# Kernel tuning notes

Hardware: AMD Instinct MI355X
Metric: run time of the kernel (lower is better)

Reference implementation:

```python
import jax, jax.numpy as jnp
import numpy as np

B, S, D_MODEL = 8, 2048, 512
G, V = 2, 320          # num_groups, num_vars
CV_DIM = 256 // G      # proj_dim // num_groups = 128
TAU = 2.0


def setup_inputs() -> dict:
    key = jax.random.key(0)
    k1, k2, k3, k4, k5 = jax.random.split(key, 5)
    hidden_states = jax.random.normal(k1, (B, S, D_MODEL), dtype=jnp.float32)
    # Linear(d_model -> G*V); store as (in, out) for direct matmul
    W = jax.random.normal(k2, (D_MODEL, G * V), dtype=jnp.float32) * (1.0 / np.sqrt(D_MODEL))
    b = jax.random.normal(k3, (G * V,), dtype=jnp.float32) * 0.01
    codevectors = jax.random.normal(k4, (1, G * V, CV_DIM), dtype=jnp.float32)
    # pre-sampled Gumbel(0,1) noise, shape (B*S*G, V)
    u = jax.random.uniform(k5, (B * S * G, V), dtype=jnp.float32,
                           minval=1e-10, maxval=1.0)
    gumbels = -jnp.log(-jnp.log(u))
    return {"hidden_states": hidden_states, "W": W, "b": b,
            "codevectors": codevectors, "gumbels": gumbels}


def reference(hidden_states, W, b, codevectors, gumbels):
    Bs, Ss, _ = hidden_states.shape
    N = Bs * Ss
    # weight projection: (B,S,D) @ (D,G*V) -> (B,S,G*V)
    logits = hidden_states @ W + b
    logits = logits.reshape(N * G, V).astype(jnp.float32)

    # gumbel-softmax, hard=True with straight-through
    y_soft = jax.nn.softmax((logits + gumbels) / TAU, axis=-1)  # (N*G, V)
    idx = jnp.argmax(y_soft, axis=-1)
    y_hard = jax.nn.one_hot(idx, V, dtype=y_soft.dtype)
    codevector_probs = y_hard - jax.lax.stop_gradient(y_soft) + y_soft

    # perplexity from the (noise-free) soft distribution
    soft_dist = jax.nn.softmax(logits.reshape(N, G, V), axis=-1)
    marginal = soft_dist.mean(axis=0)                            # (G, V)
    perplexity = jnp.exp(-jnp.sum(marginal * jnp.log(marginal + 1e-7),
                                  axis=-1)).sum()

    # codebook lookup as weighted sum (equivalent to one-hot gather)
    cv = codevectors.reshape(G, V, CV_DIM)
    probs = codevector_probs.reshape(N, G, V)
    out = jnp.einsum('ngv,gvd->ngd', probs, cv)                  # (N, G, d)
    out = out.reshape(Bs, Ss, G * CV_DIM)
    return out, perplexity
```

## Files before the change

kernel.cpp:

```cpp
#include <hip/hip_runtime.h>

#define M_ROWS 16384
#define K_DIM  512
#define N_COLS 640
#define V_CODES 320
#define CV_DIM 128
#define LSTRIDE 330

typedef _Float16 half8 __attribute__((ext_vector_type(8)));
typedef _Float16 half4v __attribute__((ext_vector_type(4)));
typedef float floatx4 __attribute__((ext_vector_type(4)));

__device__ inline void gll16(const void* g, void* l) {
    __builtin_amdgcn_global_load_lds(
        (const __attribute__((address_space(1))) void*)g,
        (__attribute__((address_space(3))) void*)l, 16, 0, 0);
}

__global__ __launch_bounds__(256)
void prepW(const float* __restrict__ W, _Float16* __restrict__ Wt,
           float* __restrict__ marginal) {
    __shared__ float tile[32][33];
    const int b = blockIdx.x, t = threadIdx.x;
    if (b == 320) {
        for (int i = t; i < 640; i += 256) marginal[i] = 0.f;
        return;
    }
    const int n0 = (b % 20) * 32, k0 = (b / 20) * 32;
    {
        const int kk = t >> 3, nn4 = (t & 7) << 2;
        const float4 w = *(const float4*)(W + (size_t)(k0 + kk) * 640 + n0 + nn4);
        tile[kk][nn4 + 0] = w.x; tile[kk][nn4 + 1] = w.y;
        tile[kk][nn4 + 2] = w.z; tile[kk][nn4 + 3] = w.w;
    }
    __syncthreads();
    {
        const int nn = t >> 3, kk4 = (t & 7) << 2;
        half4v h = {(_Float16)tile[kk4 + 0][nn], (_Float16)tile[kk4 + 1][nn],
                    (_Float16)tile[kk4 + 2][nn], (_Float16)tile[kk4 + 3][nn]};
        *(half4v*)(Wt + (size_t)(n0 + nn) * 512 + k0 + kk4) = h;
    }
}

union SMemG {
    struct { _Float16 Bs[2][320 * 32]; _Float16 As[2][64 * 32]; } g;
    _Float16 L[64 * LSTRIDE];
};

__global__ __launch_bounds__(256, 3)
void fused(const float* __restrict__ A, const _Float16* __restrict__ Bt,
           const float* __restrict__ bias, const float* __restrict__ gum,
           const float* __restrict__ cv, float* __restrict__ out,
           float* __restrict__ marginal) {
    __shared__ SMemG sm;
    __shared__ float smarg[320];
    const int t = threadIdx.x;
    const int wave = t >> 6, lane = t & 63;
    const int bm = blockIdx.x, g = blockIdx.y;
    const int mi = wave;
    const int c = lane & 15, kq = lane >> 4;

    for (int i = t; i < 320; i += 256) smarg[i] = 0.f;

    floatx4 acc[20];
#pragma unroll
    for (int nt = 0; nt < 20; ++nt) acc[nt] = (floatx4){0.f, 0.f, 0.f, 0.f};

    const int am = t >> 2, ad = t & 3;
    const int a_wr = am * 64 + ((ad ^ (am & 3)) << 4);
    const float* Aptr = A + (size_t)(bm * 64 + am) * 512 + ad * 8;

    const _Float16* Bg = Bt + (size_t)g * V_CODES * K_DIM;

    auto STAGE = [&](int buf, int k0) {
        const float4 av0 = *(const float4*)(Aptr + k0);
        const float4 av1 = *(const float4*)(Aptr + k0 + 4);
#pragma unroll
        for (int s = 0; s < 5; ++s) {
            const int q = t + 256 * s;
            const int n = q >> 2, j = q & 3;
            gll16(Bg + (size_t)n * 512 + k0 + ((j ^ (n & 3)) << 3),
                  (char*)(&sm.g.Bs[buf][0]) + q * 16);
        }
        const half8 h = {(_Float16)av0.x, (_Float16)av0.y, (_Float16)av0.z,
                         (_Float16)av0.w, (_Float16)av1.x, (_Float16)av1.y,
                         (_Float16)av1.z, (_Float16)av1.w};
        *(half8*)((char*)(&sm.g.As[buf][0]) + a_wr) = h;
    };

    STAGE(0, 0);
    __syncthreads();

    for (int kt = 0; kt < 16; ++kt) {
        const int cur = kt & 1;
        if (kt < 15) STAGE(cur ^ 1, (kt + 1) * 32);
        const int ra = mi * 16 + c;
        const half8 af = *(const half8*)((const char*)(&sm.g.As[cur][0]) +
                          ra * 64 + ((kq ^ (ra & 3)) << 4));
#pragma unroll
        for (int nt = 0; nt < 20; ++nt) {
            const int rb = nt * 16 + c;
            const half8 bf = *(const half8*)((const char*)(&sm.g.Bs[cur][0]) +
                              rb * 64 + ((kq ^ (rb & 3)) << 4));
            acc[nt] = __builtin_amdgcn_mfma_f32_16x16x32_f16(af, bf, acc[nt], 0, 0, 0);
        }
        __syncthreads();
    }

    float bcol[20];
#pragma unroll
    for (int nt = 0; nt < 20; ++nt) bcol[nt] = bias[g * V_CODES + nt * 16 + c];
#pragma unroll
    for (int rg = 0; rg < 4; ++rg) {
        const int row = mi * 16 + kq * 4 + rg;
#pragma unroll
        for (int nt = 0; nt < 20; ++nt)
            sm.L[row * LSTRIDE + nt * 16 + c] = (_Float16)(acc[nt][rg] + bcol[nt]);
    }

    float gv[4][20];
#pragma unroll
    for (int rg = 0; rg < 4; ++rg) {
        const int ntok = bm * 64 + mi * 16 + kq * 4 + rg;
        const float* gr = gum + ((size_t)ntok * 2 + g) * V_CODES + c;
#pragma unroll
        for (int nt = 0; nt < 20; ++nt) gv[rg][nt] = gr[nt * 16];
    }

    float mcontrib[20];
#pragma unroll
    for (int nt = 0; nt < 20; ++nt) mcontrib[nt] = 0.f;

#pragma unroll
    for (int rg = 0; rg < 4; ++rg) {
        const int row = mi * 16 + kq * 4 + rg;
        float lg[20];
#pragma unroll
        for (int nt = 0; nt < 20; ++nt)
            lg[nt] = (float)sm.L[row * LSTRIDE + nt * 16 + c];
        float best = -1e30f; int bidx = 0;
#pragma unroll
        for (int nt = 0; nt < 20; ++nt) {
            const float nz = lg[nt] + gv[rg][nt];
            const int v = nt * 16 + c;
            if (nz > best) { best = nz; bidx = v; }
        }
#pragma unroll
        for (int mask = 1; mask <= 8; mask <<= 1) {
            const float ob = __shfl_xor(best, mask);
            const int   oi = __shfl_xor(bidx, mask);
            if (ob > best || (ob == best && oi < bidx)) { best = ob; bidx = oi; }
        }
        float s = 0.f;
#pragma unroll
        for (int nt = 0; nt < 20; ++nt) { lg[nt] = __expf(lg[nt]); s += lg[nt]; }
#pragma unroll
        for (int mask = 1; mask <= 8; mask <<= 1) s += __shfl_xor(s, mask);
        const float inv = 1.f / s;
#pragma unroll
        for (int nt = 0; nt < 20; ++nt) mcontrib[nt] += lg[nt] * inv;
        const int ntok = bm * 64 + row;
        const float4* cvp = (const float4*)(cv + ((size_t)g * V_CODES + bidx) * CV_DIM)
                            + c * 2;
        const float4 v0 = cvp[0], v1 = cvp[1];
        float4* op = (float4*)(out + (size_t)ntok * 256 + g * CV_DIM) + c * 2;
        op[0] = v0; op[1] = v1;
    }

#pragma unroll
    for (int nt = 0; nt < 20; ++nt) {
        mcontrib[nt] += __shfl_xor(mcontrib[nt], 16);
        mcontrib[nt] += __shfl_xor(mcontrib[nt], 32);
    }
    if (lane < 16) {
#pragma unroll
        for (int nt = 0; nt < 20; ++nt)
            atomicAdd(&smarg[nt * 16 + c], mcontrib[nt]);
    }
    __syncthreads();
    for (int i = t; i < 320; i += 256)
        atomicAdd(marginal + g * V_CODES + i, smarg[i]);
}

__global__ __launch_bounds__(640)
void finalize(const float* __restrict__ marginal, float* __restrict__ perp_out) {
    __shared__ float terms[640];
    __shared__ float gsum[2];
    const int t = threadIdx.x;

    const float m = marginal[t] * (1.0f / (float)M_ROWS);
    terms[t] = -m * __logf(m + 1e-7f);
    __syncthreads();

    if (t < 128) {
        const int g = t >> 6, lane = t & 63;
        float e = 0.f;
#pragma unroll
        for (int j = 0; j < 5; ++j) e += terms[g * V_CODES + lane + 64 * j];
#pragma unroll
        for (int off = 32; off; off >>= 1) e += __shfl_down(e, off);
        if (lane == 0) gsum[g] = e;
    }
    __syncthreads();
    if (t == 0) perp_out[0] = __expf(gsum[0]) + __expf(gsum[1]);
}

extern "C" void kernel_launch(void* const* d_in, const int* in_sizes, int n_in,
                              void* d_out, int out_size, void* d_ws, size_t ws_size,
                              hipStream_t stream) {
    (void)in_sizes; (void)n_in; (void)out_size; (void)ws_size;
    const float* hs = (const float*)d_in[0];
    const float* W  = (const float*)d_in[1];
    const float* bi = (const float*)d_in[2];
    const float* cv = (const float*)d_in[3];
    const float* gu = (const float*)d_in[4];
    float* out = (float*)d_out;

    _Float16* Wt       = (_Float16*)d_ws;
    float*    marginal = (float*)(Wt + (size_t)N_COLS * K_DIM);

    prepW<<<321, 256, 0, stream>>>(W, Wt, marginal);
    fused<<<dim3(256, 2), 256, 0, stream>>>(hs, Wt, bi, gu, cv, out, marginal);
    finalize<<<1, 640, 0, stream>>>(marginal, out + (size_t)M_ROWS * 256);
}
```

Measured before the change: 50.72 us.

## Stage gumbel noise through LDS with async loads and keep logits in registers

The epilogue no longer round-trips the biased logits through an fp16 LDS buffer. It uses the accumulator registers directly, which also keeps the logits in full fp32. The gumbel noise was previously loaded with strided per-lane global reads. It is now brought into LDS in two 32-row halves with coalesced 16-byte global_load_lds transfers, and the matching two waves process each half. This is meant to fix the poorly coalesced gumbel reads and drop the LDS logit write and read. In exchange, it serializes the epilogue into two phases with extra barriers, leaving half the waves idle in each phase.

```diff
diff --git a/kernel.cpp b/kernel.cpp
--- a/kernel.cpp
+++ b/kernel.cpp
@@ -5,7 +5,6 @@
 #define N_COLS 640
 #define V_CODES 320
 #define CV_DIM 128
-#define LSTRIDE 330
 
 typedef _Float16 half8 __attribute__((ext_vector_type(8)));
 typedef _Float16 half4v __attribute__((ext_vector_type(4)));
@@ -44,7 +43,7 @@
 
 union SMemG {
     struct { _Float16 Bs[2][320 * 32]; _Float16 As[2][64 * 32]; } g;
-    _Float16 L[64 * LSTRIDE];
+    float gumL[32 * 320];
 };
 
 __global__ __launch_bounds__(256, 3)
@@ -107,77 +106,77 @@
         __syncthreads();
     }
 
-    float bcol[20];
-#pragma unroll
-    for (int nt = 0; nt < 20; ++nt) bcol[nt] = bias[g * V_CODES + nt * 16 + c];
-#pragma unroll
-    for (int rg = 0; rg < 4; ++rg) {
-        const int row = mi * 16 + kq * 4 + rg;
-#pragma unroll
-        for (int nt = 0; nt < 20; ++nt)
-            sm.L[row * LSTRIDE + nt * 16 + c] = (_Float16)(acc[nt][rg] + bcol[nt]);
-    }
-
-    float gv[4][20];
-#pragma unroll
-    for (int rg = 0; rg < 4; ++rg) {
-        const int ntok = bm * 64 + mi * 16 + kq * 4 + rg;
-        const float* gr = gum + ((size_t)ntok * 2 + g) * V_CODES + c;
-#pragma unroll
-        for (int nt = 0; nt < 20; ++nt) gv[rg][nt] = gr[nt * 16];
-    }
-
-    float mcontrib[20];
-#pragma unroll
-    for (int nt = 0; nt < 20; ++nt) mcontrib[nt] = 0.f;
-
-#pragma unroll
-    for (int rg = 0; rg < 4; ++rg) {
-        const int row = mi * 16 + kq * 4 + rg;
-        float lg[20];
-#pragma unroll
-        for (int nt = 0; nt < 20; ++nt)
-            lg[nt] = (float)sm.L[row * LSTRIDE + nt * 16 + c];
-        float best = -1e30f; int bidx = 0;
-#pragma unroll
-        for (int nt = 0; nt < 20; ++nt) {
-            const float nz = lg[nt] + gv[rg][nt];
-            const int v = nt * 16 + c;
-            if (nz > best) { best = nz; bidx = v; }
-        }
-#pragma unroll
-        for (int mask = 1; mask <= 8; mask <<= 1) {
-            const float ob = __shfl_xor(best, mask);
-            const int   oi = __shfl_xor(bidx, mask);
-            if (ob > best || (ob == best && oi < bidx)) { best = ob; bidx = oi; }
-        }
-        float s = 0.f;
-#pragma unroll
-        for (int nt = 0; nt < 20; ++nt) { lg[nt] = __expf(lg[nt]); s += lg[nt]; }
-#pragma unroll
-        for (int mask = 1; mask <= 8; mask <<= 1) s += __shfl_xor(s, mask);
-        const float inv = 1.f / s;
-#pragma unroll
-        for (int nt = 0; nt < 20; ++nt) mcontrib[nt] += lg[nt] * inv;
-        const int ntok = bm * 64 + row;
-        const float4* cvp = (const float4*)(cv + ((size_t)g * V_CODES + bidx) * CV_DIM)
-                            + c * 2;
-        const float4 v0 = cvp[0], v1 = cvp[1];
-        float4* op = (float4*)(out + (size_t)ntok * 256 + g * CV_DIM) + c * 2;
-        op[0] = v0; op[1] = v1;
-    }
-
-#pragma unroll
-    for (int nt = 0; nt < 20; ++nt) {
-        mcontrib[nt] += __shfl_xor(mcontrib[nt], 16);
-        mcontrib[nt] += __shfl_xor(mcontrib[nt], 32);
-    }
-    if (lane < 16) {
-#pragma unroll
-        for (int nt = 0; nt < 20; ++nt)
-            atomicAdd(&smarg[nt * 16 + c], mcontrib[nt]);
-    }
-    __syncthreads();
+    for (int p = 0; p < 2; ++p) {
+#pragma unroll
+        for (int s = 0; s < 10; ++s) {
+            const int q = t + 256 * s;
+            const int rip = q / 80;
+            const int cir = q % 80;
+            gll16(gum + ((size_t)(bm * 64 + p * 32 + rip) * 2 + g) * V_CODES
+                      + cir * 4,
+                  (char*)sm.gumL + q * 16);
+        }
+        __syncthreads();
+
+        if ((mi >> 1) == p) {
+            const int rbase = (mi & 1) * 16;
+            float bcol[20];
+#pragma unroll
+            for (int nt = 0; nt < 20; ++nt)
+                bcol[nt] = bias[g * V_CODES + nt * 16 + c];
+            float mcon[20];
+#pragma unroll
+            for (int nt = 0; nt < 20; ++nt) mcon[nt] = 0.f;
+
+#pragma unroll
+            for (int rg = 0; rg < 4; ++rg) {
+                const int rip = rbase + kq * 4 + rg;
+                float lg[20];
+#pragma unroll
+                for (int nt = 0; nt < 20; ++nt) lg[nt] = acc[nt][rg] + bcol[nt];
+                float best = -1e30f; int bidx = 0;
+#pragma unroll
+                for (int nt = 0; nt < 20; ++nt) {
+                    const float nz = lg[nt] + sm.gumL[rip * 320 + nt * 16 + c];
+                    const int v = nt * 16 + c;
+                    if (nz > best) { best = nz; bidx = v; }
+                }
+#pragma unroll
+                for (int mask = 1; mask <= 8; mask <<= 1) {
+                    const float ob = __shfl_xor(best, mask);
+                    const int   oi = __shfl_xor(bidx, mask);
+                    if (ob > best || (ob == best && oi < bidx)) { best = ob; bidx = oi; }
+                }
+                float s = 0.f;
+#pragma unroll
+                for (int nt = 0; nt < 20; ++nt) { lg[nt] = __expf(lg[nt]); s += lg[nt]; }
+#pragma unroll
+                for (int mask = 1; mask <= 8; mask <<= 1) s += __shfl_xor(s, mask);
+                const float inv = 1.f / s;
+#pragma unroll
+                for (int nt = 0; nt < 20; ++nt) mcon[nt] += lg[nt] * inv;
+                const int ntok = bm * 64 + mi * 16 + kq * 4 + rg;
+                const float4* cvp = (const float4*)(cv +
+                    ((size_t)g * V_CODES + bidx) * CV_DIM) + c * 2;
+                const float4 v0 = cvp[0], v1 = cvp[1];
+                float4* op = (float4*)(out + (size_t)ntok * 256 + g * CV_DIM) + c * 2;
+                op[0] = v0; op[1] = v1;
+            }
+
+#pragma unroll
+            for (int nt = 0; nt < 20; ++nt) {
+                mcon[nt] += __shfl_xor(mcon[nt], 16);
+                mcon[nt] += __shfl_xor(mcon[nt], 32);
+            }
+            if (lane < 16) {
+#pragma unroll
+                for (int nt = 0; nt < 20; ++nt)
+                    atomicAdd(&smarg[nt * 16 + c], mcon[nt]);
+            }
+        }
+        __syncthreads();
+    }
+
     for (int i = t; i < 320; i += 256)
         atomicAdd(marginal + g * V_CODES + i, smarg[i]);
 }
```

After: 128.9 us. 2.54x slower.
